# Kernel tuning notes

Hardware: AMD Instinct MI355X
Metric: run time of the kernel (lower is better)

Reference implementation:

```python
import jax, jax.numpy as jnp
import numpy as np

B = 2
D = 256          # conv_dim / d_model
NH = 8           # attention heads
NL = 3           # feature levels: res5, res4, res3 (forward iterates reversed)
NP = 4           # sampling points per head per level
NLAYERS = 6
FF = 1024
SHAPES = [(24, 24), (48, 48), (96, 96)]   # (H, W) per level in encoder order
LEN = sum(h * w for h, w in SHAPES)       # 12096
HD = D // NH


def group_norm(x, s, b, groups=32, eps=1e-5):
    Bb, C, H, W = x.shape
    xr = x.reshape(Bb, groups, C // groups, H, W)
    m = xr.mean((2, 3, 4), keepdims=True)
    v = xr.var((2, 3, 4), keepdims=True)
    xr = (xr - m) * jax.lax.rsqrt(v + eps)
    return xr.reshape(Bb, C, H, W) * s[:, None, None] + b[:, None, None]


def layer_norm(x, s, b, eps=1e-5):
    m = x.mean(-1, keepdims=True)
    v = x.var(-1, keepdims=True)
    return (x - m) * jax.lax.rsqrt(v + eps) * s + b


def pos_embed_sine(H, W):
    # PositionEmbeddingSine(num_pos_feats=D//2, normalize=True), mask=None
    num = D // 2
    eps = 1e-6
    scale = 2.0 * np.pi
    y = (jnp.arange(1, H + 1, dtype=jnp.float32) / (H + eps)) * scale
    x = (jnp.arange(1, W + 1, dtype=jnp.float32) / (W + eps)) * scale
    dim_t = 10000.0 ** (2.0 * (jnp.arange(num) // 2).astype(jnp.float32) / num)
    def enc(v):
        p = v[:, None] / dim_t
        return jnp.stack([jnp.sin(p[:, 0::2]), jnp.cos(p[:, 1::2])], -1).reshape(v.shape[0], num)
    pe_y, pe_x = enc(y), enc(x)
    pos = jnp.concatenate([
        jnp.broadcast_to(pe_y[:, None, :], (H, W, num)),
        jnp.broadcast_to(pe_x[None, :, :], (H, W, num))], -1)
    return pos.transpose(2, 0, 1)  # [D, H, W]


def ms_deform_sample(value, loc, attn):
    # value [B,LEN,NH,HD]; loc [B,LEN,NH,NL,NP,2] in [0,1] (x,y); attn [B,LEN,NH,NL,NP]
    # Equivalent to grid_sample(bilinear, padding=zeros, align_corners=False) per level.
    out = jnp.zeros((B * NH, LEN, HD), jnp.float32)
    start = 0
    for lvl, (H, W) in enumerate(SHAPES):
        v = value[:, start:start + H * W].transpose(0, 2, 1, 3).reshape(B * NH, H * W, HD)
        l = loc[:, :, :, lvl].transpose(0, 2, 1, 3, 4).reshape(B * NH, LEN * NP, 2)
        x = l[..., 0] * W - 0.5
        y = l[..., 1] * H - 0.5
        x0f = jnp.floor(x); y0f = jnp.floor(y)
        wx = x - x0f; wy = y - y0f
        x0 = x0f.astype(jnp.int32); y0 = y0f.astype(jnp.int32)
        def gather(yi, xi):
            valid = (xi >= 0) & (xi < W) & (yi >= 0) & (yi < H)
            idx = jnp.clip(yi, 0, H - 1) * W + jnp.clip(xi, 0, W - 1)
            g = jnp.take_along_axis(v, idx[..., None], axis=1)
            return g * valid[..., None]
        s = (gather(y0, x0) * ((1 - wx) * (1 - wy))[..., None]
             + gather(y0, x0 + 1) * (wx * (1 - wy))[..., None]
             + gather(y0 + 1, x0) * ((1 - wx) * wy)[..., None]
             + gather(y0 + 1, x0 + 1) * (wx * wy)[..., None])
        w = attn[:, :, :, lvl].transpose(0, 2, 1, 3).reshape(B * NH, LEN * NP)
        out = out + (s * w[..., None]).reshape(B * NH, LEN, NP, HD).sum(2)
        start += H * W
    return out.reshape(B, NH, LEN, HD).transpose(0, 2, 1, 3).reshape(B, LEN, D)


def upsample_bilinear(x, Ho, Wo):
    # F.interpolate(mode='bilinear', align_corners=False)
    Bb, C, H, W = x.shape
    ys = jnp.maximum((jnp.arange(Ho, dtype=jnp.float32) + 0.5) * (H / Ho) - 0.5, 0.0)
    xs = jnp.maximum((jnp.arange(Wo, dtype=jnp.float32) + 0.5) * (W / Wo) - 0.5, 0.0)
    y0 = jnp.floor(ys).astype(jnp.int32); wy = ys - y0
    x0 = jnp.floor(xs).astype(jnp.int32); wx = xs - x0
    y1 = jnp.minimum(y0 + 1, H - 1); x1 = jnp.minimum(x0 + 1, W - 1)
    r = x[:, :, y0, :] * (1 - wy)[None, None, :, None] + x[:, :, y1, :] * wy[None, None, :, None]
    return r[:, :, :, x0] * (1 - wx)[None, None, None, :] + r[:, :, :, x1] * wx[None, None, None, :]


def conv1x1(x, w):
    return jnp.einsum('bchw,oc->bohw', x, w)


def _forward(res2, res3, res4, res5,
             pw5, pb5, gs5, gb5, pw4, pb4, gs4, gb4, pw3, pb3, gs3, gb3,
             level_embed, off_w, off_b, aw_w, aw_b, val_w, val_b, out_w, out_b,
             ln1_s, ln1_b, ffn1_w, ffn1_b, ffn2_w, ffn2_b, ln2_s, ln2_b,
             lat_w, lat_gs, lat_gb, fpn_w, fpn_gs, fpn_gb):
    feats = [res5, res4, res3]  # transformer_in_features reversed (coarse -> fine)
    projs = [(pw5, pb5, gs5, gb5), (pw4, pb4, gs4, gb4), (pw3, pb3, gs3, gb3)]
    src_list, pos_list = [], []
    for f, (pw, pb, gs, gb) in zip(feats, projs):
        s = group_norm(conv1x1(f, pw) + pb[:, None, None], gs, gb)
        src_list.append(s.reshape(B, D, -1).transpose(0, 2, 1))
        pos_list.append(pos_embed_sine(f.shape[2], f.shape[3]))
    src = jnp.concatenate(src_list, axis=1)  # [B, LEN, D]
    pos = jnp.concatenate([p.reshape(D, -1).T + level_embed[i]
                           for i, p in enumerate(pos_list)], axis=0)[None]  # [1, LEN, D]
    # reference points (x, y), valid_ratios == 1 (no padding masks)
    refs = []
    for H, W in SHAPES:
        gy, gx = jnp.meshgrid((jnp.arange(H, dtype=jnp.float32) + 0.5) / H,
                              (jnp.arange(W, dtype=jnp.float32) + 0.5) / W, indexing='ij')
        refs.append(jnp.stack([gx.ravel(), gy.ravel()], -1))
    ref_pts = jnp.broadcast_to(jnp.concatenate(refs, 0)[None, :, None, :], (B, LEN, NL, 2))
    norm_wh = jnp.array([[W, H] for H, W in SHAPES], jnp.float32)  # offset normalizer (x=W, y=H)
    for l in range(NLAYERS):
        q = src + pos
        value = (src @ val_w[l] + val_b[l]).reshape(B, LEN, NH, HD)
        off = (q @ off_w[l] + off_b[l]).reshape(B, LEN, NH, NL, NP, 2)
        aw = jax.nn.softmax((q @ aw_w[l] + aw_b[l]).reshape(B, LEN, NH, NL * NP), -1)
        aw = aw.reshape(B, LEN, NH, NL, NP)
        loc = ref_pts[:, :, None, :, None, :] + off / norm_wh[None, None, None, :, None, :]
        attn = ms_deform_sample(value, loc, aw) @ out_w[l] + out_b[l]
        src = layer_norm(src + attn, ln1_s[l], ln1_b[l])
        h = jax.nn.relu(src @ ffn1_w[l] + ffn1_b[l]) @ ffn2_w[l] + ffn2_b[l]
        src = layer_norm(src + h, ln2_s[l], ln2_b[l])
    outs, start = [], 0
    for H, W in SHAPES:
        outs.append(src[:, start:start + H * W].transpose(0, 2, 1).reshape(B, D, H, W))
        start += H * W
    # FPN: single lateral/output level (res2)
    lat = group_norm(conv1x1(res2, lat_w), lat_gs, lat_gb)
    y = lat + upsample_bilinear(outs[-1], lat.shape[2], lat.shape[3])
    y = jax.lax.conv_general_dilated(y, fpn_w, (1, 1), 'SAME',
                                     dimension_numbers=('NCHW', 'OIHW', 'NCHW'))
    y = jax.nn.relu(group_norm(y, fpn_gs, fpn_gb))
    # returns (out[-1], out[0], multi_scale_features...) = (fpn, y_res5, y_res5, y_res4, y_res3)
    return y, outs[0], outs[1], outs[2]


def setup_inputs():
    ks = jax.random.split(jax.random.key(0), 40)
    def rn(i, shape, s=0.02):
        return jax.random.normal(ks[i], shape, jnp.float32) * s
    inp = {}
    inp['res2'] = jax.random.normal(ks[0], (B, 256, 192, 192), jnp.float32)
    inp['res3'] = jax.random.normal(ks[1], (B, 512, 96, 96), jnp.float32)
    inp['res4'] = jax.random.normal(ks[2], (B, 1024, 48, 48), jnp.float32)
    inp['res5'] = jax.random.normal(ks[3], (B, 2048, 24, 24), jnp.float32)
    for name, cin, i in [('5', 2048, 4), ('4', 1024, 5), ('3', 512, 6)]:
        inp['pw' + name] = rn(i, (D, cin))
        inp['pb' + name] = jnp.zeros((D,), jnp.float32)
        inp['gs' + name] = jnp.ones((D,), jnp.float32)
        inp['gb' + name] = jnp.zeros((D,), jnp.float32)
    inp['level_embed'] = rn(7, (NL, D), 1.0)
    inp['off_w'] = rn(8, (NLAYERS, D, NH * NL * NP * 2))
    inp['off_b'] = rn(9, (NLAYERS, NH * NL * NP * 2), 0.5)
    inp['aw_w'] = rn(10, (NLAYERS, D, NH * NL * NP))
    inp['aw_b'] = jnp.zeros((NLAYERS, NH * NL * NP), jnp.float32)
    inp['val_w'] = rn(11, (NLAYERS, D, D))
    inp['val_b'] = jnp.zeros((NLAYERS, D), jnp.float32)
    inp['out_w'] = rn(12, (NLAYERS, D, D))
    inp['out_b'] = jnp.zeros((NLAYERS, D), jnp.float32)
    inp['ln1_s'] = jnp.ones((NLAYERS, D), jnp.float32)
    inp['ln1_b'] = jnp.zeros((NLAYERS, D), jnp.float32)
    inp['ffn1_w'] = rn(13, (NLAYERS, D, FF))
    inp['ffn1_b'] = jnp.zeros((NLAYERS, FF), jnp.float32)
    inp['ffn2_w'] = rn(14, (NLAYERS, FF, D))
    inp['ffn2_b'] = jnp.zeros((NLAYERS, D), jnp.float32)
    inp['ln2_s'] = jnp.ones((NLAYERS, D), jnp.float32)
    inp['ln2_b'] = jnp.zeros((NLAYERS, D), jnp.float32)
    inp['lat_w'] = rn(15, (D, 256))
    inp['lat_gs'] = jnp.ones((D,), jnp.float32)
    inp['lat_gb'] = jnp.zeros((D,), jnp.float32)
    inp['fpn_w'] = rn(16, (D, D, 3, 3))
    inp['fpn_gs'] = jnp.ones((D,), jnp.float32)
    inp['fpn_gb'] = jnp.zeros((D,), jnp.float32)
    return inp


def reference(res2, res3, res4, res5,
              pw5, pb5, gs5, gb5, pw4, pb4, gs4, gb4, pw3, pb3, gs3, gb3,
              level_embed, off_w, off_b, aw_w, aw_b, val_w, val_b, out_w, out_b,
              ln1_s, ln1_b, ffn1_w, ffn1_b, ffn2_w, ffn2_b, ln2_s, ln2_b,
              lat_w, lat_gs, lat_gb, fpn_w, fpn_gs, fpn_gb):
    return _forward(res2, res3, res4, res5,
                    pw5, pb5, gs5, gb5, pw4, pb4, gs4, gb4, pw3, pb3, gs3, gb3,
                    level_embed, off_w, off_b, aw_w, aw_b, val_w, val_b, out_w, out_b,
                    ln1_s, ln1_b, ffn1_w, ffn1_b, ffn2_w, ffn2_b, ln2_s, ln2_b,
                    lat_w, lat_gs, lat_gb, fpn_w, fpn_gs, fpn_gb)
```

## Files before the change

kernel.cpp:

```cpp
#include <hip/hip_runtime.h>
#include <math.h>

#define NLEN 12096
#define BB 2

typedef __bf16 bhalf;
typedef bhalf bh8 __attribute__((ext_vector_type(8)));
typedef bhalf bh4 __attribute__((ext_vector_type(4)));
typedef float f32x4 __attribute__((ext_vector_type(4)));

__device__ __forceinline__ int swz(int row) { return (row >> 1) & 3; }

__device__ __forceinline__ int xcd_swz(int id, int nwg) {
  int q = nwg >> 3, r = nwg & 7;
  int xcd = id & 7, pos = id >> 3;
  int base = (xcd < r) ? xcd * (q + 1) : r * (q + 1) + (xcd - r) * q;
  return base + pos;
}

#define GLOAD_LDS16(g, l) \
  __builtin_amdgcn_global_load_lds( \
      (const __attribute__((address_space(1))) unsigned int*)(g), \
      (__attribute__((address_space(3))) unsigned int*)(l), 16, 0, 0)

template<int BNF>
__global__ __launch_bounds__(256) void bgemm_t_kernel(
    const bhalf* __restrict__ A, const bhalf* __restrict__ Bt,
    const float* __restrict__ bias, void* __restrict__ Cout,
    int M, int N, int K, long long sA, long long sB, long long sC,
    int outBf16, int relu)
{
  constexpr int BN = BNF * 16;
  constexpr int ROWS = 128 + BN;
  constexpr int UNITS = ROWS * 4;
  constexpr int ITERS = (UNITS + 255) / 256;
  constexpr int NFR = BNF / 2;
  const int gx = gridDim.x, gy = gridDim.y;
  const int nwg = gx * gy * gridDim.z;
  int flat = (blockIdx.z * gy + blockIdx.y) * gx + blockIdx.x;
  int logical = xcd_swz(flat, nwg);
  const int bz = logical / (gx * gy);
  int rem = logical - bz * gx * gy;
  const int by = rem / gx;
  const int bx = rem - by * gx;

  A += bz * sA; Bt += bz * sB;
  const int m0 = by * 128, n0 = bx * BN;
  __shared__ __align__(16) bhalf Ls[ROWS * 32];
  const int t = threadIdx.x;
  const int lane = t & 63;
  const int w = t >> 6;
  const int wbase = t & 192;
  const int wm = (w >> 1) * 64, wn = (w & 1) * (BN / 2);
  const int fr = lane & 15, fg = lane >> 4;
  f32x4 acc[4][NFR] = {};
  for (int k0 = 0; k0 < K; k0 += 32) {
#pragma unroll
    for (int j = 0; j < ITERS; ++j) {
      int u = t + j * 256;
      if (UNITS % 256 == 0 || u < UNITS) {
        int row = u >> 2, up = u & 3;
        int kcg = ((up ^ swz(row)) * 8);
        const bhalf* gsrc;
        if (row < 128) {
          int m = m0 + row; m = (m < M) ? m : (M - 1);
          gsrc = A + (long long)m * K + k0 + kcg;
        } else {
          int n = n0 + row - 128; n = (n < N) ? n : (N - 1);
          gsrc = Bt + (long long)n * K + k0 + kcg;
        }
        GLOAD_LDS16(gsrc, Ls + (long long)(wbase + j * 256) * 8);
      }
    }
    __syncthreads();
    bh8 af[4], bf[NFR];
#pragma unroll
    for (int mi = 0; mi < 4; ++mi) {
      int r = wm + mi * 16 + fr;
      af[mi] = *(const bh8*)(Ls + r * 32 + ((fg ^ swz(r)) * 8));
    }
#pragma unroll
    for (int ni = 0; ni < NFR; ++ni) {
      int r = 128 + wn + ni * 16 + fr;
      bf[ni] = *(const bh8*)(Ls + r * 32 + ((fg ^ swz(r)) * 8));
    }
#pragma unroll
    for (int mi = 0; mi < 4; ++mi)
#pragma unroll
      for (int ni = 0; ni < NFR; ++ni)
        acc[mi][ni] = __builtin_amdgcn_mfma_f32_16x16x32_bf16(af[mi], bf[ni], acc[mi][ni], 0, 0, 0);
    __syncthreads();
  }
  float* Cf = (float*)Cout + bz * sC;
  bhalf* Cb = (bhalf*)Cout + bz * sC;
#pragma unroll
  for (int mi = 0; mi < 4; ++mi) {
#pragma unroll
    for (int r = 0; r < 4; ++r) {
      int m = m0 + wm + mi * 16 + fg * 4 + r;
      if (m >= M) continue;
#pragma unroll
      for (int ni = 0; ni < NFR; ++ni) {
        int n = n0 + wn + ni * 16 + fr;
        if (n >= N) continue;
        float v = acc[mi][ni][r];
        if (bias) v += bias[n];
        if (relu) v = fmaxf(v, 0.f);
        if (outBf16) Cb[(long long)m * N + n] = (bhalf)v;
        else         Cf[(long long)m * N + n] = v;
      }
    }
  }
}

__global__ __launch_bounds__(256) void bgemm_ln_kernel(
    const bhalf* __restrict__ A, const bhalf* __restrict__ Bt,
    const float* __restrict__ bias,
    bhalf* __restrict__ srcb, bhalf* __restrict__ qbOut,
    const float* __restrict__ pos,
    const float* __restrict__ ls, const float* __restrict__ lb,
    int M, int K)
{
  const int nwg = gridDim.x;
  const int bid = xcd_swz(blockIdx.x, nwg);
  const int m0 = bid * 32;
  __shared__ __align__(16) bhalf Ls[288 * 32];
  __shared__ float shS[32][2], shQ[32][2];
  const int t = threadIdx.x;
  const int lane = t & 63;
  const int w = t >> 6;
  const int wbase = t & 192;
  const int wm = (w >> 1) * 16, wn = (w & 1) * 128;
  const int fr = lane & 15, fg = lane >> 4;
  f32x4 acc[8] = {};
  for (int k0 = 0; k0 < K; k0 += 32) {
#pragma unroll
    for (int j = 0; j < 5; ++j) {
      int u = t + j * 256;
      if (u < 1152) {
        int row = u >> 2, up = u & 3;
        int kcg = ((up ^ swz(row)) * 8);
        const bhalf* gsrc = (row < 32)
            ? (A + (long long)(m0 + row) * K + k0 + kcg)
            : (Bt + (long long)(row - 32) * K + k0 + kcg);
        GLOAD_LDS16(gsrc, Ls + (long long)(wbase + j * 256) * 8);
      }
    }
    __syncthreads();
    bh8 af, bf[8];
    {
      int r = wm + fr;
      af = *(const bh8*)(Ls + r * 32 + ((fg ^ swz(r)) * 8));
    }
#pragma unroll
    for (int ni = 0; ni < 8; ++ni) {
      int r = 32 + wn + ni * 16 + fr;
      bf[ni] = *(const bh8*)(Ls + r * 32 + ((fg ^ swz(r)) * 8));
    }
#pragma unroll
    for (int ni = 0; ni < 8; ++ni)
      acc[ni] = __builtin_amdgcn_mfma_f32_16x16x32_bf16(af, bf[ni], acc[ni], 0, 0, 0);
    __syncthreads();
  }
#pragma unroll
  for (int r = 0; r < 4; ++r) {
    int rt = wm + fg * 4 + r;
    long long gm = m0 + rt;
    float s = 0.f, q = 0.f;
#pragma unroll
    for (int ni = 0; ni < 8; ++ni) {
      int col = wn + ni * 16 + fr;
      float v = acc[ni][r] + bias[col] + (float)srcb[gm * 256 + col];
      acc[ni][r] = v;
      s += v; q = fmaf(v, v, q);
    }
#pragma unroll
    for (int o = 1; o < 16; o <<= 1) { s += __shfl_xor(s, o); q += __shfl_xor(q, o); }
    if (fr == 0) { shS[rt][w & 1] = s; shQ[rt][w & 1] = q; }
  }
  __syncthreads();
#pragma unroll
  for (int r = 0; r < 4; ++r) {
    int rt = wm + fg * 4 + r;
    long long gm = m0 + rt;
    float S = shS[rt][0] + shS[rt][1];
    float Q = shQ[rt][0] + shQ[rt][1];
    float mean = S * (1.f / 256.f);
    float var = Q * (1.f / 256.f) - mean * mean;
    float rstd = rsqrtf(var + 1e-5f);
    int prow = (int)(gm % NLEN);
#pragma unroll
    for (int ni = 0; ni < 8; ++ni) {
      int col = wn + ni * 16 + fr;
      float y = (acc[ni][r] - mean) * rstd * ls[col] + lb[col];
      srcb[gm * 256 + col] = (bhalf)y;
      if (qbOut) qbOut[gm * 256 + col] = (bhalf)(y + pos[(long long)prow * 256 + col]);
    }
  }
}

__global__ __launch_bounds__(256) void bgemm_conv_kernel(
    const bhalf* __restrict__ Ab, const bhalf* __restrict__ Bt,
    bhalf* __restrict__ Cout)
{
  const int gx = gridDim.x, gy = gridDim.y;
  const int nwg = gx * gy * gridDim.z;
  int flat = (blockIdx.z * gy + blockIdx.y) * gx + blockIdx.x;
  int logical = xcd_swz(flat, nwg);
  const int bz = logical / (gx * gy);
  int rem = logical - bz * gx * gy;
  const int by = rem / gx;
  const int bx = rem - by * gx;

  const bhalf* Apad = Ab + (long long)bz * 37636 * 256;
  const int m0 = by * 128, n0 = bx * 128;
  __shared__ __align__(16) bhalf As[128 * 32];
  __shared__ __align__(16) bhalf Bs[128 * 32];
  const int t = threadIdx.x;
  const int lane = t & 63;
  const int w = t >> 6;
  const int wbase = t & 192;
  const int wm = (w >> 1) * 64, wn = (w & 1) * 64;
  const int fr = lane & 15, fg = lane >> 4;
  int rowA[2], py[2], px[2], kcg[2];
#pragma unroll
  for (int j = 0; j < 2; ++j) {
    int id = t + j * 256;
    rowA[j] = id >> 2;
    kcg[j] = (((id & 3) ^ swz(rowA[j])) * 8);
    int m = m0 + rowA[j];
    py[j] = m / 192; px[j] = m % 192;
  }
  f32x4 acc[4][4] = {};
  for (int s = 0; s < 72; ++s) {
    const int cib = s / 9, tap = s % 9;
    const int ty = tap / 3, tx = tap % 3;
#pragma unroll
    for (int j = 0; j < 2; ++j) {
      GLOAD_LDS16(Apad + ((long long)(py[j] + ty) * 194 + px[j] + tx) * 256 + cib * 32 + kcg[j],
                  As + (wbase + j * 256) * 8);
      GLOAD_LDS16(Bt + (long long)(n0 + rowA[j]) * 2304 + s * 32 + kcg[j],
                  Bs + (wbase + j * 256) * 8);
    }
    __syncthreads();
    bh8 af[4], bf[4];
#pragma unroll
    for (int mi = 0; mi < 4; ++mi) {
      int r = wm + mi * 16 + fr;
      af[mi] = *(const bh8*)(As + r * 32 + ((fg ^ swz(r)) * 8));
    }
#pragma unroll
    for (int ni = 0; ni < 4; ++ni) {
      int r = wn + ni * 16 + fr;
      bf[ni] = *(const bh8*)(Bs + r * 32 + ((fg ^ swz(r)) * 8));
    }
#pragma unroll
    for (int mi = 0; mi < 4; ++mi)
#pragma unroll
      for (int ni = 0; ni < 4; ++ni)
        acc[mi][ni] = __builtin_amdgcn_mfma_f32_16x16x32_bf16(af[mi], bf[ni], acc[mi][ni], 0, 0, 0);
    __syncthreads();
  }
  bhalf* Cb = Cout + (long long)bz * 36864 * 256;
#pragma unroll
  for (int mi = 0; mi < 4; ++mi)
#pragma unroll
    for (int r = 0; r < 4; ++r) {
      int m = m0 + wm + mi * 16 + fg * 4 + r;
#pragma unroll
      for (int ni = 0; ni < 4; ++ni) {
        int n = n0 + wn + ni * 16 + fr;
        Cb[(long long)m * 256 + n] = (bhalf)acc[mi][ni][r];
      }
    }
}

__global__ void wprep_t_kernel(
    const float* __restrict__ s0, const float* __restrict__ s1,
    const float* __restrict__ s2, const float* __restrict__ s3,
    const float* __restrict__ s4, const float* __restrict__ s5,
    bhalf* __restrict__ d0, bhalf* __restrict__ d1, bhalf* __restrict__ d2,
    bhalf* __restrict__ d3, bhalf* __restrict__ d4, bhalf* __restrict__ d5)
{
  const int KdA[6]  = {256, 256, 256, 256, 256, 1024};
  const int NdA[6]  = {256, 192, 96, 256, 1024, 256};
  const long long zdA[6] = {65536, 73728, 73728, 65536, 262144, 262144};
  const int cum[6]  = {384, 672, 816, 1200, 2736, 4272};
  int blk = blockIdx.x;
  int seg = 0;
#pragma unroll
  for (int i = 0; i < 6; ++i) if (blk >= cum[i]) seg = i + 1;
  int base = (seg == 0) ? 0 : cum[seg - 1];
  int idx = blk - base;
  const float* Wsrc = (seg == 0) ? s0 : (seg == 1) ? s1 : (seg == 2) ? s2
                    : (seg == 3) ? s3 : (seg == 4) ? s4 : s5;
  bhalf* out = (seg == 0) ? d0 : (seg == 1) ? d1 : (seg == 2) ? d2
             : (seg == 3) ? d3 : (seg == 4) ? d4 : d5;
  int Kd = KdA[seg], Nd = NdA[seg];
  int nx = Nd / 32, ny = Kd / 32;
  int z = idx / (nx * ny);
  int r = idx - z * nx * ny;
  int ky = r / nx, nxi = r - ky * nx;
  __shared__ float tile[32][33];
  long long zi = (long long)z * Kd * Nd;
  long long zo = (long long)z * zdA[seg];
  int n0 = nxi * 32, k0 = ky * 32;
#pragma unroll
  for (int j = 0; j < 4; ++j) {
    int kk = threadIdx.y + 8 * j;
    tile[kk][threadIdx.x] = Wsrc[zi + (long long)(k0 + kk) * Nd + n0 + threadIdx.x];
  }
  __syncthreads();
#pragma unroll
  for (int j = 0; j < 4; ++j) {
    int nn = threadIdx.y + 8 * j;
    out[zo + (long long)(n0 + nn) * Kd + k0 + threadIdx.x] = (bhalf)tile[threadIdx.x][nn];
  }
}

__global__ void wprep_m_kernel(
    const float* __restrict__ fpn_w, bhalf* __restrict__ fpnT,
    const float* __restrict__ pw5, bhalf* __restrict__ pwb5,
    const float* __restrict__ pw4, bhalf* __restrict__ pwb4,
    const float* __restrict__ pw3, bhalf* __restrict__ pwb3,
    const float* __restrict__ lat_w, bhalf* __restrict__ latwb,
    const float* __restrict__ ob, const float* __restrict__ ab,
    float* __restrict__ offaw_b)
{
  int blk = blockIdx.x, t = threadIdx.x;
  if (blk < 2304) {
    int o = blk * 256 + t;
    int co = o / 2304, r = o % 2304;
    int cib = r / 288, rr = r % 288, tap = rr >> 5, cil = rr & 31;
    int ci = cib * 32 + cil;
    fpnT[o] = (bhalf)fpn_w[(co * 256 + ci) * 9 + tap];
  } else if (blk < 4352) {
    int i = (blk - 2304) * 256 + t; pwb5[i] = (bhalf)pw5[i];
  } else if (blk < 5376) {
    int i = (blk - 4352) * 256 + t; pwb4[i] = (bhalf)pw4[i];
  } else if (blk < 5888) {
    int i = (blk - 5376) * 256 + t; pwb3[i] = (bhalf)pw3[i];
  } else if (blk < 6144) {
    int i = (blk - 5888) * 256 + t; latwb[i] = (bhalf)lat_w[i];
  } else {
    int i = (blk - 6144) * 256 + t;
    if (i < 6 * 288) {
      int l = i / 288, c = i % 288;
      offaw_b[i] = (c < 192) ? ob[l * 192 + c] : ab[l * 96 + c - 192];
    }
  }
}

__global__ void tfeat_kernel(const float* __restrict__ Fsrc, bhalf* __restrict__ out,
                             int Ci, int HW)
{
  __shared__ float tile[32][33];
  long long zo = (long long)blockIdx.z * Ci * HW;
  int hw0 = blockIdx.x * 32, c0 = blockIdx.y * 32;
#pragma unroll
  for (int j = 0; j < 4; ++j) {
    int cc = threadIdx.y + 8 * j;
    tile[cc][threadIdx.x] = Fsrc[zo + (long long)(c0 + cc) * HW + hw0 + threadIdx.x];
  }
  __syncthreads();
#pragma unroll
  for (int j = 0; j < 4; ++j) {
    int hh = threadIdx.y + 8 * j;
    out[zo + (long long)(hw0 + hh) * Ci + c0 + threadIdx.x] = (bhalf)tile[threadIdx.x][hh];
  }
}

__global__ void border_zero_kernel(bhalf* __restrict__ latb)
{
  int idx = blockIdx.x * 256 + threadIdx.x;
  int total = BB * 4 * 194;
  if (idx >= total) return;
  int b = idx / (4 * 194);
  int r = idx - b * 4 * 194;
  int strip = r / 194, p = r % 194;
  int y, x;
  if (strip == 0)      { y = 0;   x = p; }
  else if (strip == 1) { y = 193; x = p; }
  else if (strip == 2) { y = p;   x = 0; }
  else                 { y = p;   x = 193; }
  uint4* dst = (uint4*)(latb + ((long long)b * 37636 + (long long)y * 194 + x) * 256);
#pragma unroll
  for (int j = 0; j < 32; ++j) dst[j] = make_uint4(0u, 0u, 0u, 0u);
}

__global__ void pos_kernel(float* __restrict__ pos, const float* __restrict__ level_embed)
{
  int i = blockIdx.x, c = threadIdx.x;
  int lvl, Wq, loc;
  if (i < 576)       { lvl = 0; Wq = 24; loc = i; }
  else if (i < 2880) { lvl = 1; Wq = 48; loc = i - 576; }
  else               { lvl = 2; Wq = 96; loc = i - 2880; }
  int h = loc / Wq, wcol = loc % Wq;
  int cc = c & 127;
  float coord = (c < 128) ? (float)(h + 1) : (float)(wcol + 1);
  float denom = (float)Wq + 1e-6f;
  float v = coord / denom * 6.28318530717958647692f;
  float tp = powf(10000.0f, (float)(cc & ~1) * (1.0f / 128.0f));
  float ang = v / tp;
  float val = (cc & 1) ? cosf(ang) : sinf(ang);
  pos[(long long)i * 256 + c] = val + level_embed[lvl * 256 + c];
}

__global__ __launch_bounds__(256) void gn_part_kernel(const void* __restrict__ X,
    float* __restrict__ part, int HW, int isBf16, int nch)
{
  const int b = blockIdx.y, ch = blockIdx.x;
  const int rows = (HW + nch - 1) / nch;
  const int r0 = ch * rows;
  const int r1 = min(r0 + rows, HW);
  const int cg = threadIdx.x & 31;
  const int ro = threadIdx.x >> 5;
  float s = 0.f, s2 = 0.f;
  if (isBf16) {
    const bhalf* p = (const bhalf*)X + (long long)b * HW * 256 + cg * 8;
    for (int r = r0 + ro; r < r1; r += 8) {
      bh8 v = *(const bh8*)(p + (long long)r * 256);
#pragma unroll
      for (int j = 0; j < 8; ++j) { float f = (float)v[j]; s += f; s2 = fmaf(f, f, s2); }
    }
  } else {
    const float* p = (const float*)X + (long long)b * HW * 256 + cg * 8;
    for (int r = r0 + ro; r < r1; r += 8) {
      f32x4 v0 = *(const f32x4*)(p + (long long)r * 256);
      f32x4 v1 = *(const f32x4*)(p + (long long)r * 256 + 4);
#pragma unroll
      for (int j = 0; j < 4; ++j) { s += v0[j]; s2 = fmaf(v0[j], v0[j], s2); }
#pragma unroll
      for (int j = 0; j < 4; ++j) { s += v1[j]; s2 = fmaf(v1[j], v1[j], s2); }
    }
  }
  __shared__ float sh[2][8][32];
  sh[0][ro][cg] = s; sh[1][ro][cg] = s2;
  __syncthreads();
  if (threadIdx.x < 32) {
    float S = 0.f, S2 = 0.f;
#pragma unroll
    for (int k = 0; k < 8; ++k) { S += sh[0][k][threadIdx.x]; S2 += sh[1][k][threadIdx.x]; }
    long long o = ((long long)(b * 32 + threadIdx.x) * nch + ch) * 2;
    part[o] = S; part[o + 1] = S2;
  }
}

__global__ __launch_bounds__(64) void gn_fin_kernel(const float* __restrict__ part,
    float* __restrict__ stats, int nch, int HW)
{
  const int bg = blockIdx.x;
  float s = 0.f, s2 = 0.f;
  for (int i = threadIdx.x; i < nch; i += 64) {
    long long o = ((long long)bg * nch + i) * 2;
    s += part[o]; s2 += part[o + 1];
  }
#pragma unroll
  for (int o = 32; o > 0; o >>= 1) { s += __shfl_down(s, o); s2 += __shfl_down(s2, o); }
  if (threadIdx.x == 0) {
    float inv = 1.f / (float)(HW * 8);
    float mean = s * inv;
    float var = s2 * inv - mean * mean;
    stats[bg * 2] = mean;
    stats[bg * 2 + 1] = rsqrtf(var + 1e-5f);
  }
}

__global__ void gn_apply_rm_kernel(const bhalf* __restrict__ T, const float* __restrict__ stats,
    const float* __restrict__ gs, const float* __restrict__ gb,
    bhalf* __restrict__ srcb, bhalf* __restrict__ qb,
    const float* __restrict__ pos, int HW, int startRow)
{
  long long idx = (long long)blockIdx.x * 256 + threadIdx.x;
  int c = threadIdx.x & 255;
  long long row = idx >> 8;
  int b = (int)(row / HW);
  long long hw = row - (long long)b * HW;
  int g = c >> 3;
  float v = (float)T[idx];
  v = (v - stats[(b * 32 + g) * 2]) * stats[(b * 32 + g) * 2 + 1] * gs[c] + gb[c];
  long long pr = (startRow + hw) * 256 + c;
  long long o = (long long)b * NLEN * 256 + pr;
  srcb[o] = (bhalf)v;
  qb[o] = (bhalf)(v + pos[pr]);
}

__global__ __launch_bounds__(256) void deform_kernel(const bhalf* __restrict__ value,
    const bhalf* __restrict__ offaw, bhalf* __restrict__ out)
{
  const int t = threadIdx.x;
  const int q = t >> 5;
  const int sub = t & 31;
  const int bi = blockIdx.x * 8 + q;
  const int i = bi % NLEN;
  const int bbase = bi - i;
  const int c0 = sub * 8;
  const int head = sub >> 2;
  int loc, Wq;
  if (i < 576)       { Wq = 24; loc = i; }
  else if (i < 2880) { Wq = 48; loc = i - 576; }
  else               { Wq = 96; loc = i - 2880; }
  const float rx = ((loc % Wq) + 0.5f) / (float)Wq;
  const float ry = ((loc / Wq) + 0.5f) / (float)Wq;
  const bhalf* offp = offaw + (long long)bi * 288 + head * 24;
  const bhalf* awp  = offaw + (long long)bi * 288 + 192 + head * 12;
  float aw[12];
  float ssum = 0.f;
#pragma unroll
  for (int j = 0; j < 12; ++j) { aw[j] = __expf((float)awp[j]); ssum += aw[j]; }
  const float sinv = 1.f / ssum;
  float acc[8] = {};
  const int starts[3] = {0, 576, 2880};
  const int Ls[3] = {24, 48, 96};
#pragma unroll
  for (int l = 0; l < 3; ++l) {
    const int Wl = Ls[l];
    const float fW = (float)Wl;
    const bhalf* vb = value + (long long)(bbase + starts[l]) * 256 + c0;
#pragma unroll
    for (int p = 0; p < 4; ++p) {
      const float ox = (float)offp[l * 8 + p * 2], oy = (float)offp[l * 8 + p * 2 + 1];
      const float a = aw[l * 4 + p] * sinv;
      const float x = (rx + ox / fW) * fW - 0.5f;
      const float y = (ry + oy / fW) * fW - 0.5f;
      const float x0f = floorf(x), y0f = floorf(y);
      const float wx = x - x0f, wy = y - y0f;
      const int x0 = (int)x0f, y0 = (int)y0f;
      const int x1 = x0 + 1, y1 = y0 + 1;
      const bool xv0 = (x0 >= 0) & (x0 < Wl);
      const bool xv1 = (x1 >= 0) & (x1 < Wl);
      const bool yv0 = (y0 >= 0) & (y0 < Wl);
      const bool yv1 = (y1 >= 0) & (y1 < Wl);
      const int cx0 = min(max(x0, 0), Wl - 1), cx1 = min(max(x1, 0), Wl - 1);
      const int cy0 = min(max(y0, 0), Wl - 1), cy1 = min(max(y1, 0), Wl - 1);
      const float w00 = (xv0 && yv0) ? (1.f - wx) * (1.f - wy) * a : 0.f;
      const float w01 = (xv1 && yv0) ? wx * (1.f - wy) * a : 0.f;
      const float w10 = (xv0 && yv1) ? (1.f - wx) * wy * a : 0.f;
      const float w11 = (xv1 && yv1) ? wx * wy * a : 0.f;
      const bh8 g00 = *(const bh8*)(vb + (cy0 * Wl + cx0) * 256);
      const bh8 g01 = *(const bh8*)(vb + (cy0 * Wl + cx1) * 256);
      const bh8 g10 = *(const bh8*)(vb + (cy1 * Wl + cx0) * 256);
      const bh8 g11 = *(const bh8*)(vb + (cy1 * Wl + cx1) * 256);
#pragma unroll
      for (int e = 0; e < 8; ++e)
        acc[e] = fmaf(w00, (float)g00[e], fmaf(w01, (float)g01[e],
                 fmaf(w10, (float)g10[e], fmaf(w11, (float)g11[e], acc[e]))));
    }
  }
  bh8 o;
#pragma unroll
  for (int e = 0; e < 8; ++e) o[e] = (bhalf)acc[e];
  *(bh8*)(out + (long long)bi * 256 + c0) = o;
}

__global__ void transpose_out_kernel(const bhalf* __restrict__ srcb,
    float* __restrict__ out0, float* __restrict__ out1, float* __restrict__ out2)
{
  int blk = blockIdx.x;
  int HW, startRow;
  float* out;
  if (blk < 288)       { HW = 576;  startRow = 0;    out = out0; }
  else if (blk < 1440) { HW = 2304; startRow = 576;  out = out1; blk -= 288; }
  else                 { HW = 9216; startRow = 2880; out = out2; blk -= 1440; }
  int nx = HW / 32;
  int bx = blk % nx; int r = blk / nx;
  int cy = r % 8; int b = r / 8;
  __shared__ float tile[32][33];
  int w0 = bx * 32, c0 = cy * 32;
#pragma unroll
  for (int j = 0; j < 4; ++j) {
    int wl = threadIdx.y + 8 * j;
    tile[wl][threadIdx.x] =
        (float)srcb[((long long)b * NLEN + startRow + w0 + wl) * 256 + c0 + threadIdx.x];
  }
  __syncthreads();
#pragma unroll
  for (int j = 0; j < 4; ++j) {
    int cl = threadIdx.y + 8 * j;
    out[((long long)b * 256 + c0 + cl) * HW + w0 + threadIdx.x] = tile[threadIdx.x][cl];
  }
}

__global__ void lat_finish_rm_kernel(const bhalf* __restrict__ lat, const float* __restrict__ stats,
    const float* __restrict__ gs, const float* __restrict__ gb,
    const bhalf* __restrict__ srcb, bhalf* __restrict__ latb)
{
  long long idx = (long long)blockIdx.x * 256 + threadIdx.x;
  int c = threadIdx.x & 255;
  long long row = idx >> 8;
  int b = (int)(row / 36864);
  int p = (int)(row - (long long)b * 36864);
  int y = p / 192, x = p % 192;
  int g = c >> 3;
  float v = (float)lat[idx];
  v = (v - stats[(b * 32 + g) * 2]) * stats[(b * 32 + g) * 2 + 1] * gs[c] + gb[c];
  float ys = fmaxf(y * 0.5f - 0.25f, 0.f);
  float xs = fmaxf(x * 0.5f - 0.25f, 0.f);
  int y0 = (int)ys; float wy = ys - (float)y0; int y1 = min(y0 + 1, 95);
  int x0 = (int)xs; float wx = xs - (float)x0; int x1 = min(x0 + 1, 95);
  const bhalf* sp = srcb + ((long long)b * NLEN + 2880) * 256 + c;
  float r0 = (float)sp[(long long)(y0 * 96 + x0) * 256] * (1.f - wx)
           + (float)sp[(long long)(y0 * 96 + x1) * 256] * wx;
  float r1 = (float)sp[(long long)(y1 * 96 + x0) * 256] * (1.f - wx)
           + (float)sp[(long long)(y1 * 96 + x1) * 256] * wx;
  latb[((long long)b * 37636 + (long long)(y + 1) * 194 + (x + 1)) * 256 + c]
      = (bhalf)(v + r0 * (1.f - wy) + r1 * wy);
}

__global__ void gn_relu_tr_kernel(const bhalf* __restrict__ convC, const float* __restrict__ stats,
    const float* __restrict__ gs, const float* __restrict__ gb, float* __restrict__ Y)
{
  __shared__ float tile[32][33];
  int b = blockIdx.z;
  int hw0 = blockIdx.x * 32, c0 = blockIdx.y * 32;
#pragma unroll
  for (int j = 0; j < 4; ++j) {
    int hwl = threadIdx.y + 8 * j;
    int c = c0 + threadIdx.x;
    int g = c >> 3;
    float v = (float)convC[((long long)b * 36864 + hw0 + hwl) * 256 + c];
    v = (v - stats[(b * 32 + g) * 2]) * stats[(b * 32 + g) * 2 + 1] * gs[c] + gb[c];
    tile[hwl][threadIdx.x] = fmaxf(v, 0.f);
  }
  __syncthreads();
#pragma unroll
  for (int j = 0; j < 4; ++j) {
    int cl = threadIdx.y + 8 * j;
    Y[((long long)b * 256 + c0 + cl) * 36864 + hw0 + threadIdx.x] = tile[threadIdx.x][cl];
  }
}

extern "C" void kernel_launch(void* const* d_in, const int* in_sizes, int n_in,
                              void* d_out, int out_size, void* d_ws, size_t ws_size,
                              hipStream_t stream)
{
  const float* res2 = (const float*)d_in[0];
  const float* res3 = (const float*)d_in[1];
  const float* res4 = (const float*)d_in[2];
  const float* res5 = (const float*)d_in[3];
  const float* pw[3]  = {(const float*)d_in[4],  (const float*)d_in[8],  (const float*)d_in[12]};
  const float* pb[3]  = {(const float*)d_in[5],  (const float*)d_in[9],  (const float*)d_in[13]};
  const float* gss[3] = {(const float*)d_in[6],  (const float*)d_in[10], (const float*)d_in[14]};
  const float* gbb[3] = {(const float*)d_in[7],  (const float*)d_in[11], (const float*)d_in[15]};
  const float* level_embed = (const float*)d_in[16];
  const float* off_w = (const float*)d_in[17];
  const float* off_b = (const float*)d_in[18];
  const float* aw_w  = (const float*)d_in[19];
  const float* aw_b  = (const float*)d_in[20];
  const float* val_w = (const float*)d_in[21];
  const float* val_b = (const float*)d_in[22];
  const float* out_w = (const float*)d_in[23];
  const float* out_b = (const float*)d_in[24];
  const float* ln1_s = (const float*)d_in[25];
  const float* ln1_b = (const float*)d_in[26];
  const float* ffn1_w = (const float*)d_in[27];
  const float* ffn1_b = (const float*)d_in[28];
  const float* ffn2_w = (const float*)d_in[29];
  const float* ffn2_b = (const float*)d_in[30];
  const float* ln2_s = (const float*)d_in[31];
  const float* ln2_b = (const float*)d_in[32];
  const float* lat_w = (const float*)d_in[33];
  const float* lat_gs = (const float*)d_in[34];
  const float* lat_gb = (const float*)d_in[35];
  const float* fpn_w = (const float*)d_in[36];
  const float* fpn_gs = (const float*)d_in[37];
  const float* fpn_gb = (const float*)d_in[38];

  char* W = (char*)d_ws;
  float* pos   = (float*)(W + 24772608LL);
  bhalf* tmpb  = (bhalf*)(W + 37158912LL);
  bhalf* srcb  = (bhalf*)(W + 61931520LL);
  bhalf* wreg  = (bhalf*)(W + 74317824LL);
  float* stats = (float*)(W + 86212608LL);
  float* part  = (float*)(W + 86213120LL);
  float* offaw_b = (float*)(W + 86278656LL);
  char*  U     = W + 86286848LL;

  bhalf* valT   = wreg + 0;
  bhalf* offawT = wreg + 393216;
  bhalf* outT   = wreg + 835584;
  bhalf* f1T    = wreg + 1228800;
  bhalf* f2T    = wreg + 2801664;
  bhalf* pwb5   = wreg + 4374528;
  bhalf* pwb4   = wreg + 4898816;
  bhalf* pwb3   = wreg + 5160960;
  bhalf* latwb  = wreg + 5292032;
  bhalf* fpnT   = wreg + 5357568;

  bhalf* qb      = (bhalf*)(U + 0);
  bhalf* valueb  = (bhalf*)(U + 12386304LL);
  bhalf* sampb   = (bhalf*)(U + 24772608LL);
  bhalf* offbuf  = (bhalf*)(U + 37158912LL);
  bhalf* hbuf    = (bhalf*)(U + 65028096LL);
  bhalf* featT   = (bhalf*)(U + 24772608LL);
  bhalf* res2T   = (bhalf*)(U + 0);
  bhalf* latbf   = (bhalf*)(U + 37748736LL);
  bhalf* latb    = (bhalf*)(U + 75497472LL);

  float* Yout = (float*)d_out;
  float* out0 = Yout + 18874368LL;
  float* out1 = Yout + 19169280LL;
  float* out2 = Yout + 20348928LL;

  const int M = BB * NLEN;

  wprep_t_kernel<<<dim3(4272), dim3(32, 8), 0, stream>>>(
      val_w, off_w, aw_w, out_w, ffn1_w, ffn2_w,
      valT, offawT, offawT + 192 * 256, outT, f1T, f2T);
  wprep_m_kernel<<<dim3(6151), dim3(256), 0, stream>>>(
      fpn_w, fpnT, pw[0], pwb5, pw[1], pwb4, pw[2], pwb3,
      lat_w, latwb, off_b, aw_b, offaw_b);

  pos_kernel<<<dim3(NLEN), dim3(256), 0, stream>>>(pos, level_embed);

  const float* feats[3] = {res5, res4, res3};
  const bhalf* pwbs[3] = {pwb5, pwb4, pwb3};
  const int cins[3] = {2048, 1024, 512};
  const int HWs[3] = {576, 2304, 9216};
  const int startsHost[3] = {0, 576, 2880};
  const int nchs[3] = {16, 64, 128};
  for (int lvl = 0; lvl < 3; ++lvl) {
    int HW = HWs[lvl], cin = cins[lvl], nch = nchs[lvl];
    tfeat_kernel<<<dim3(HW / 32, cin / 32, BB), dim3(32, 8), 0, stream>>>(feats[lvl], featT, cin, HW);
    bgemm_t_kernel<4><<<dim3(4, (HW + 127) / 128, BB), dim3(256), 0, stream>>>(
        featT, pwbs[lvl], pb[lvl], tmpb, HW, 256, cin,
        (long long)HW * cin, 0LL, (long long)HW * 256, 1, 0);
    gn_part_kernel<<<dim3(nch, BB), dim3(256), 0, stream>>>(tmpb, part, HW, 1, nch);
    gn_fin_kernel<<<dim3(64), dim3(64), 0, stream>>>(part, stats, nch, HW);
    gn_apply_rm_kernel<<<dim3(BB * HW), dim3(256), 0, stream>>>(
        tmpb, stats, gss[lvl], gbb[lvl], srcb, qb, pos, HW, startsHost[lvl]);
  }

  for (int l = 0; l < 6; ++l) {
    bgemm_t_kernel<4><<<dim3(4, M / 128, 1), dim3(256), 0, stream>>>(
        srcb, valT + (long long)l * 65536, val_b + l * 256, valueb,
        M, 256, 256, 0LL, 0LL, 0LL, 1, 0);
    bgemm_t_kernel<6><<<dim3(3, M / 128, 1), dim3(256), 0, stream>>>(
        qb, offawT + (long long)l * 73728, offaw_b + l * 288, offbuf,
        M, 288, 256, 0LL, 0LL, 0LL, 1, 0);
    deform_kernel<<<dim3(M / 8), dim3(256), 0, stream>>>(valueb, offbuf, sampb);
    bgemm_ln_kernel<<<dim3(M / 32), dim3(256), 0, stream>>>(
        sampb, outT + (long long)l * 65536, out_b + l * 256,
        srcb, nullptr, pos, ln1_s + l * 256, ln1_b + l * 256, M, 256);
    bgemm_t_kernel<8><<<dim3(8, M / 128, 1), dim3(256), 0, stream>>>(
        srcb, f1T + (long long)l * 262144, ffn1_b + l * 1024, hbuf,
        M, 1024, 256, 0LL, 0LL, 0LL, 1, 1);
    bgemm_ln_kernel<<<dim3(M / 32), dim3(256), 0, stream>>>(
        hbuf, f2T + (long long)l * 262144, ffn2_b + l * 256,
        srcb, qb, pos, ln2_s + l * 256, ln2_b + l * 256, M, 1024);
  }

  transpose_out_kernel<<<dim3(6048), dim3(32, 8), 0, stream>>>(srcb, out0, out1, out2);

  tfeat_kernel<<<dim3(1152, 8, BB), dim3(32, 8), 0, stream>>>(res2, res2T, 256, 36864);
  bgemm_t_kernel<4><<<dim3(4, 288, BB), dim3(256), 0, stream>>>(
      res2T, latwb, nullptr, latbf, 36864, 256, 256,
      36864LL * 256, 0LL, 36864LL * 256, 1, 0);
  gn_part_kernel<<<dim3(128, BB), dim3(256), 0, stream>>>(latbf, part, 36864, 1, 128);
  gn_fin_kernel<<<dim3(64), dim3(64), 0, stream>>>(part, stats, 128, 36864);
  border_zero_kernel<<<dim3((BB * 4 * 194 + 255) / 256), dim3(256), 0, stream>>>(latb);
  lat_finish_rm_kernel<<<dim3(73728), dim3(256), 0, stream>>>(latbf, stats, lat_gs, lat_gb, srcb, latb);
  bgemm_conv_kernel<<<dim3(2, 288, BB), dim3(256), 0, stream>>>(latb, fpnT, latbf);
  gn_part_kernel<<<dim3(128, BB), dim3(256), 0, stream>>>(latbf, part, 36864, 1, 128);
  gn_fin_kernel<<<dim3(64), dim3(64), 0, stream>>>(part, stats, 128, 36864);
  gn_relu_tr_kernel<<<dim3(1152, 8, BB), dim3(32, 8), 0, stream>>>(latbf, stats, fpn_gs, fpn_gb, Yout);
}
```

Before: 1.531 ms.

## Fuse deformable sampling into output-projection GEMM with residual LayerNorm

Merges the deformable-attention sampling kernel with the following output-projection GEMM plus residual-add and LayerNorm. Each block samples 32 rows straight into a swizzled LDS A-tile and then runs the MFMA GEMM and LN epilogue, so the sampled tensor no longer makes a round trip through global memory and one launch per layer goes away. The cost is lower occupancy from the larger LDS use, and the gather phase and GEMM phase no longer overlap across separate kernels.

```diff
diff --git a/kernel.cpp b/kernel.cpp
--- a/kernel.cpp
+++ b/kernel.cpp
@@ -109,6 +109,154 @@
         if (outBf16) Cb[(long long)m * N + n] = (bhalf)v;
         else         Cf[(long long)m * N + n] = v;
       }
+    }
+  }
+}
+
+__global__ __launch_bounds__(256) void deform_ln_kernel(
+    const bhalf* __restrict__ value, const bhalf* __restrict__ offaw,
+    const bhalf* __restrict__ Bt, const float* __restrict__ bias,
+    bhalf* __restrict__ srcb,
+    const float* __restrict__ ls, const float* __restrict__ lb, int M)
+{
+  const int nwg = gridDim.x;
+  const int bid = xcd_swz(blockIdx.x, nwg);
+  const int m0 = bid * 32;
+  __shared__ __align__(16) bhalf ALds[32 * 256];
+  __shared__ __align__(16) bhalf BLds[256 * 32];
+  __shared__ float shS[32][2], shQ[32][2];
+  const int t = threadIdx.x;
+  const int lane = t & 63;
+  const int w = t >> 6;
+  const int wbase = t & 192;
+  const int fr = lane & 15, fg = lane >> 4;
+
+  const int starts[3] = {0, 576, 2880};
+  const int Lsz[3] = {24, 48, 96};
+#pragma unroll
+  for (int pass = 0; pass < 4; ++pass) {
+    const int q = pass * 8 + (t >> 5);
+    const int sub = t & 31;
+    const int bi = m0 + q;
+    const int i = bi % NLEN;
+    const int bbase = bi - i;
+    const int c0 = sub * 8;
+    const int head = sub >> 2;
+    int loc, Wq;
+    if (i < 576)       { Wq = 24; loc = i; }
+    else if (i < 2880) { Wq = 48; loc = i - 576; }
+    else               { Wq = 96; loc = i - 2880; }
+    const float rx = ((loc % Wq) + 0.5f) / (float)Wq;
+    const float ry = ((loc / Wq) + 0.5f) / (float)Wq;
+    const bhalf* offp = offaw + (long long)bi * 288 + head * 24;
+    const bhalf* awp  = offaw + (long long)bi * 288 + 192 + head * 12;
+    float aw[12];
+    float ssum = 0.f;
+#pragma unroll
+    for (int j = 0; j < 12; ++j) { aw[j] = __expf((float)awp[j]); ssum += aw[j]; }
+    const float sinv = 1.f / ssum;
+    float acc[8] = {};
+#pragma unroll
+    for (int l = 0; l < 3; ++l) {
+      const int Wl = Lsz[l];
+      const float fW = (float)Wl;
+      const bhalf* vb = value + (long long)(bbase + starts[l]) * 256 + c0;
+#pragma unroll
+      for (int p = 0; p < 4; ++p) {
+        const float ox = (float)offp[l * 8 + p * 2], oy = (float)offp[l * 8 + p * 2 + 1];
+        const float a = aw[l * 4 + p] * sinv;
+        const float x = (rx + ox / fW) * fW - 0.5f;
+        const float y = (ry + oy / fW) * fW - 0.5f;
+        const float x0f = floorf(x), y0f = floorf(y);
+        const float wx = x - x0f, wy = y - y0f;
+        const int x0 = (int)x0f, y0 = (int)y0f;
+        const int x1 = x0 + 1, y1 = y0 + 1;
+        const bool xv0 = (x0 >= 0) & (x0 < Wl);
+        const bool xv1 = (x1 >= 0) & (x1 < Wl);
+        const bool yv0 = (y0 >= 0) & (y0 < Wl);
+        const bool yv1 = (y1 >= 0) & (y1 < Wl);
+        const int cx0 = min(max(x0, 0), Wl - 1), cx1 = min(max(x1, 0), Wl - 1);
+        const int cy0 = min(max(y0, 0), Wl - 1), cy1 = min(max(y1, 0), Wl - 1);
+        const float w00 = (xv0 && yv0) ? (1.f - wx) * (1.f - wy) * a : 0.f;
+        const float w01 = (xv1 && yv0) ? wx * (1.f - wy) * a : 0.f;
+        const float w10 = (xv0 && yv1) ? (1.f - wx) * wy * a : 0.f;
+        const float w11 = (xv1 && yv1) ? wx * wy * a : 0.f;
+        const bh8 g00 = *(const bh8*)(vb + (cy0 * Wl + cx0) * 256);
+        const bh8 g01 = *(const bh8*)(vb + (cy0 * Wl + cx1) * 256);
+        const bh8 g10 = *(const bh8*)(vb + (cy1 * Wl + cx0) * 256);
+        const bh8 g11 = *(const bh8*)(vb + (cy1 * Wl + cx1) * 256);
+#pragma unroll
+        for (int e = 0; e < 8; ++e)
+          acc[e] = fmaf(w00, (float)g00[e], fmaf(w01, (float)g01[e],
+                   fmaf(w10, (float)g10[e], fmaf(w11, (float)g11[e], acc[e]))));
+      }
+    }
+    bh8 o;
+#pragma unroll
+    for (int e = 0; e < 8; ++e) o[e] = (bhalf)acc[e];
+    const int kc = c0 >> 5;
+    const int up = (c0 >> 3) & 3;
+    *(bh8*)(ALds + kc * 1024 + q * 32 + ((up ^ swz(q)) * 8)) = o;
+  }
+  __syncthreads();
+
+  const int wm = (w >> 1) * 16, wn = (w & 1) * 128;
+  f32x4 acc[8] = {};
+  for (int k0 = 0; k0 < 256; k0 += 32) {
+#pragma unroll
+    for (int j = 0; j < 4; ++j) {
+      int u = t + j * 256;
+      int row = u >> 2, up = u & 3;
+      int kcg = ((up ^ swz(row)) * 8);
+      GLOAD_LDS16(Bt + (long long)row * 256 + k0 + kcg, BLds + (long long)(wbase + j * 256) * 8);
+    }
+    __syncthreads();
+    bh8 af, bf[8];
+    {
+      int r = wm + fr;
+      af = *(const bh8*)(ALds + (k0 >> 5) * 1024 + r * 32 + ((fg ^ swz(r)) * 8));
+    }
+#pragma unroll
+    for (int ni = 0; ni < 8; ++ni) {
+      int r = wn + ni * 16 + fr;
+      bf[ni] = *(const bh8*)(BLds + r * 32 + ((fg ^ swz(r)) * 8));
+    }
+#pragma unroll
+    for (int ni = 0; ni < 8; ++ni)
+      acc[ni] = __builtin_amdgcn_mfma_f32_16x16x32_bf16(af, bf[ni], acc[ni], 0, 0, 0);
+    __syncthreads();
+  }
+#pragma unroll
+  for (int r = 0; r < 4; ++r) {
+    int rt = wm + fg * 4 + r;
+    long long gm = m0 + rt;
+    float s = 0.f, q = 0.f;
+#pragma unroll
+    for (int ni = 0; ni < 8; ++ni) {
+      int col = wn + ni * 16 + fr;
+      float v = acc[ni][r] + bias[col] + (float)srcb[gm * 256 + col];
+      acc[ni][r] = v;
+      s += v; q = fmaf(v, v, q);
+    }
+#pragma unroll
+    for (int o = 1; o < 16; o <<= 1) { s += __shfl_xor(s, o); q += __shfl_xor(q, o); }
+    if (fr == 0) { shS[rt][w & 1] = s; shQ[rt][w & 1] = q; }
+  }
+  __syncthreads();
+#pragma unroll
+  for (int r = 0; r < 4; ++r) {
+    int rt = wm + fg * 4 + r;
+    long long gm = m0 + rt;
+    float S = shS[rt][0] + shS[rt][1];
+    float Q = shQ[rt][0] + shQ[rt][1];
+    float mean = S * (1.f / 256.f);
+    float var = Q * (1.f / 256.f) - mean * mean;
+    float rstd = rsqrtf(var + 1e-5f);
+#pragma unroll
+    for (int ni = 0; ni < 8; ++ni) {
+      int col = wn + ni * 16 + fr;
+      float y = (acc[ni][r] - mean) * rstd * ls[col] + lb[col];
+      srcb[gm * 256 + col] = (bhalf)y;
     }
   }
 }
@@ -483,74 +631,6 @@
   long long o = (long long)b * NLEN * 256 + pr;
   srcb[o] = (bhalf)v;
   qb[o] = (bhalf)(v + pos[pr]);
-}
-
-__global__ __launch_bounds__(256) void deform_kernel(const bhalf* __restrict__ value,
-    const bhalf* __restrict__ offaw, bhalf* __restrict__ out)
-{
-  const int t = threadIdx.x;
-  const int q = t >> 5;
-  const int sub = t & 31;
-  const int bi = blockIdx.x * 8 + q;
-  const int i = bi % NLEN;
-  const int bbase = bi - i;
-  const int c0 = sub * 8;
-  const int head = sub >> 2;
-  int loc, Wq;
-  if (i < 576)       { Wq = 24; loc = i; }
-  else if (i < 2880) { Wq = 48; loc = i - 576; }
-  else               { Wq = 96; loc = i - 2880; }
-  const float rx = ((loc % Wq) + 0.5f) / (float)Wq;
-  const float ry = ((loc / Wq) + 0.5f) / (float)Wq;
-  const bhalf* offp = offaw + (long long)bi * 288 + head * 24;
-  const bhalf* awp  = offaw + (long long)bi * 288 + 192 + head * 12;
-  float aw[12];
-  float ssum = 0.f;
-#pragma unroll
-  for (int j = 0; j < 12; ++j) { aw[j] = __expf((float)awp[j]); ssum += aw[j]; }
-  const float sinv = 1.f / ssum;
-  float acc[8] = {};
-  const int starts[3] = {0, 576, 2880};
-  const int Ls[3] = {24, 48, 96};
-#pragma unroll
-  for (int l = 0; l < 3; ++l) {
-    const int Wl = Ls[l];
-    const float fW = (float)Wl;
-    const bhalf* vb = value + (long long)(bbase + starts[l]) * 256 + c0;
-#pragma unroll
-    for (int p = 0; p < 4; ++p) {
-      const float ox = (float)offp[l * 8 + p * 2], oy = (float)offp[l * 8 + p * 2 + 1];
-      const float a = aw[l * 4 + p] * sinv;
-      const float x = (rx + ox / fW) * fW - 0.5f;
-      const float y = (ry + oy / fW) * fW - 0.5f;
-      const float x0f = floorf(x), y0f = floorf(y);
-      const float wx = x - x0f, wy = y - y0f;
-      const int x0 = (int)x0f, y0 = (int)y0f;
-      const int x1 = x0 + 1, y1 = y0 + 1;
-      const bool xv0 = (x0 >= 0) & (x0 < Wl);
-      const bool xv1 = (x1 >= 0) & (x1 < Wl);
-      const bool yv0 = (y0 >= 0) & (y0 < Wl);
-      const bool yv1 = (y1 >= 0) & (y1 < Wl);
-      const int cx0 = min(max(x0, 0), Wl - 1), cx1 = min(max(x1, 0), Wl - 1);
-      const int cy0 = min(max(y0, 0), Wl - 1), cy1 = min(max(y1, 0), Wl - 1);
-      const float w00 = (xv0 && yv0) ? (1.f - wx) * (1.f - wy) * a : 0.f;
-      const float w01 = (xv1 && yv0) ? wx * (1.f - wy) * a : 0.f;
-      const float w10 = (xv0 && yv1) ? (1.f - wx) * wy * a : 0.f;
-      const float w11 = (xv1 && yv1) ? wx * wy * a : 0.f;
-      const bh8 g00 = *(const bh8*)(vb + (cy0 * Wl + cx0) * 256);
-      const bh8 g01 = *(const bh8*)(vb + (cy0 * Wl + cx1) * 256);
-      const bh8 g10 = *(const bh8*)(vb + (cy1 * Wl + cx0) * 256);
-      const bh8 g11 = *(const bh8*)(vb + (cy1 * Wl + cx1) * 256);
-#pragma unroll
-      for (int e = 0; e < 8; ++e)
-        acc[e] = fmaf(w00, (float)g00[e], fmaf(w01, (float)g01[e],
-                 fmaf(w10, (float)g10[e], fmaf(w11, (float)g11[e], acc[e]))));
-    }
-  }
-  bh8 o;
-#pragma unroll
-  for (int e = 0; e < 8; ++e) o[e] = (bhalf)acc[e];
-  *(bh8*)(out + (long long)bi * 256 + c0) = o;
 }
 
 __global__ void transpose_out_kernel(const bhalf* __restrict__ srcb,
@@ -689,7 +769,6 @@
 
   bhalf* qb      = (bhalf*)(U + 0);
   bhalf* valueb  = (bhalf*)(U + 12386304LL);
-  bhalf* sampb   = (bhalf*)(U + 24772608LL);
   bhalf* offbuf  = (bhalf*)(U + 37158912LL);
   bhalf* hbuf    = (bhalf*)(U + 65028096LL);
   bhalf* featT   = (bhalf*)(U + 24772608LL);
@@ -738,10 +817,9 @@
     bgemm_t_kernel<6><<<dim3(3, M / 128, 1), dim3(256), 0, stream>>>(
         qb, offawT + (long long)l * 73728, offaw_b + l * 288, offbuf,
         M, 288, 256, 0LL, 0LL, 0LL, 1, 0);
-    deform_kernel<<<dim3(M / 8), dim3(256), 0, stream>>>(valueb, offbuf, sampb);
-    bgemm_ln_kernel<<<dim3(M / 32), dim3(256), 0, stream>>>(
-        sampb, outT + (long long)l * 65536, out_b + l * 256,
-        srcb, nullptr, pos, ln1_s + l * 256, ln1_b + l * 256, M, 256);
+    deform_ln_kernel<<<dim3(M / 32), dim3(256), 0, stream>>>(
+        valueb, offbuf, outT + (long long)l * 65536, out_b + l * 256,
+        srcb, ln1_s + l * 256, ln1_b + l * 256, M);
     bgemm_t_kernel<8><<<dim3(8, M / 128, 1), dim3(256), 0, stream>>>(
         srcb, f1T + (long long)l * 262144, ffn1_b + l * 1024, hbuf,
         M, 1024, 256, 0LL, 0LL, 0LL, 1, 1);
```

After: 1.957 ms. 1.28x slower.
